# Optimization experiments

Measured on AMD Instinct MI355X. Metric: run time of the kernel, lower is better.

## Reference

```python
import jax, jax.numpy as jnp
import numpy as np

B, S, D, H, L, V = 32, 100, 1024, 16, 2, 32000
DF = 4 * D
EPS_LN = 1e-5
EPS_Q = 1e-6


def _ln(x, scale, bias):
    mu = jnp.mean(x, axis=-1, keepdims=True)
    var = jnp.mean(jnp.square(x - mu), axis=-1, keepdims=True)
    return (x - mu) * jax.lax.rsqrt(var + EPS_LN) * scale + bias


def setup_inputs() -> dict:
    key = jax.random.key(0)
    ks = jax.random.split(key, 20)
    sd = 0.02
    inp = {
        "x": jax.random.randint(ks[0], (B, S), 0, V),
        "emb": jax.random.normal(ks[1], (V, D), jnp.float32) * sd,
        "pos_emb": jax.random.normal(ks[2], (100, D), jnp.float32) * sd,
        "qkv_w": jax.random.normal(ks[3], (L, 3 * D, D), jnp.float32) * sd,
        "qkv_b": jnp.zeros((L, 3 * D), jnp.float32),
        "out_w": jax.random.normal(ks[4], (L, D, D), jnp.float32) * sd,
        "out_b": jnp.zeros((L, D), jnp.float32),
        "ln1_s": jnp.ones((L, D), jnp.float32),
        "ln1_b": jnp.zeros((L, D), jnp.float32),
        "ff1_w": jax.random.normal(ks[5], (L, DF, D), jnp.float32) * sd,
        "ff1_b": jnp.zeros((L, DF), jnp.float32),
        "ff2_w": jax.random.normal(ks[6], (L, D, DF), jnp.float32) * sd,
        "ff2_b": jnp.zeros((L, D), jnp.float32),
        "ln2_s": jnp.ones((L, D), jnp.float32),
        "ln2_b": jnp.zeros((L, D), jnp.float32),
        "dec_w": jax.random.normal(ks[7], (V, D), jnp.float32) * sd,
        "dec_b": jnp.zeros((V,), jnp.float32),
    }
    return inp


def reference(x, emb, pos_emb, qkv_w, qkv_b, out_w, out_b, ln1_s, ln1_b,
              ff1_w, ff1_b, ff2_w, ff2_b, ln2_s, ln2_b, dec_w, dec_b):
    hd = D // H
    h = emb[x] + pos_emb[:S][None, :, :]  # [B,S,D]
    for l in range(L):
        qkv = h @ qkv_w[l].T + qkv_b[l]  # [B,S,3D]
        q, k, v = jnp.split(qkv, 3, axis=-1)
        q = q.reshape(B, S, H, hd).transpose(0, 2, 1, 3)
        k = k.reshape(B, S, H, hd).transpose(0, 2, 1, 3)
        v = v.reshape(B, S, H, hd).transpose(0, 2, 1, 3)
        scores = jnp.einsum('bhqd,bhkd->bhqk', q, k) / jnp.sqrt(jnp.float32(hd))
        attn = jax.nn.softmax(scores, axis=-1)
        ctx = jnp.einsum('bhqk,bhkd->bhqd', attn, v)
        ctx = ctx.transpose(0, 2, 1, 3).reshape(B, S, D)
        attn_out = ctx @ out_w[l].T + out_b[l]
        h = _ln(h + attn_out, ln1_s[l], ln1_b[l])  # post-norm
        ff = jax.nn.gelu(h @ ff1_w[l].T + ff1_b[l], approximate=False) @ ff2_w[l].T + ff2_b[l]
        h = _ln(h + ff, ln2_s[l], ln2_b[l])
    # Ternary decoder (faithful to the original pack/unpack semantics:
    # packed code = q+1; unpack adds x when code==1 (q==0) and subtracts when
    # code==2 (q==+1), i.e. effective weight = {q==0: +1, q==+1: -1, q==-1: 0}).
    g = jnp.mean(jnp.abs(dec_w))
    wq = jnp.clip(jnp.round(dec_w / (g + EPS_Q)), -1.0, 1.0)
    w_eff = jnp.where(wq == 0.0, 1.0, jnp.where(wq == 1.0, -1.0, 0.0)).astype(jnp.float32)
    return h @ w_eff.T + dec_b  # [B,S,V]
```

## Files before the change

### kernel.cpp

```cpp
#include <hip/hip_runtime.h>
#include <hip/hip_bf16.h>
#include <math.h>

#define B_ 32
#define S_ 100
#define D_ 1024
#define H_ 16
#define L_ 2
#define V_ 32000
#define DF_ 4096
#define HD_ 64
#define MPAD 3328

typedef __bf16 bf16x8 __attribute__((ext_vector_type(8)));
typedef float f32x4 __attribute__((ext_vector_type(4)));

__device__ __forceinline__ void async_copy16(const void* g, void* l) {
  __builtin_amdgcn_global_load_lds((const __attribute__((address_space(1))) void*)g,
                                   (__attribute__((address_space(3))) void*)l, 16, 0, 0);
}

__global__ void absmean_kernel(const float* __restrict__ w, double* __restrict__ out) {
  const long long n4 = (long long)V_ * D_ / 4;
  double s = 0.0;
  long long stride = (long long)gridDim.x * blockDim.x;
  for (long long i = (long long)blockIdx.x * blockDim.x + threadIdx.x; i < n4; i += stride) {
    float4 v = ((const float4*)w)[i];
    s += (double)fabsf(v.x) + (double)fabsf(v.y) + (double)fabsf(v.z) + (double)fabsf(v.w);
  }
#pragma unroll
  for (int off = 32; off > 0; off >>= 1) s += __shfl_down(s, off);
  __shared__ double sm[4];
  int lane = threadIdx.x & 63, wv = threadIdx.x >> 6;
  if (lane == 0) sm[wv] = s;
  __syncthreads();
  if (threadIdx.x == 0) atomicAdd(out, sm[0] + sm[1] + sm[2] + sm[3]);
}

__global__ void quantize_kernel(const float* __restrict__ w, const double* __restrict__ gsum,
                                __hip_bfloat16* __restrict__ q) {
  const long long n4 = (long long)V_ * D_ / 4;
  double g = (*gsum) / ((double)V_ * D_) + 1e-6;
  long long stride = (long long)gridDim.x * blockDim.x;
  for (long long i = (long long)blockIdx.x * blockDim.x + threadIdx.x; i < n4; i += stride) {
    float4 v = ((const float4*)w)[i];
    union { __hip_bfloat16 h[4]; uint2 u; } o;
    float vv[4] = {v.x, v.y, v.z, v.w};
#pragma unroll
    for (int j = 0; j < 4; ++j) {
      double r = rint((double)vv[j] / g);
      r = fmin(1.0, fmax(-1.0, r));
      float w_eff = (r == 0.0) ? 1.0f : ((r == 1.0) ? -1.0f : 0.0f);
      o.h[j] = __float2bfloat16(w_eff);
    }
    ((uint2*)q)[i] = o.u;
  }
}

__global__ void cast_kernel(const float* __restrict__ in, __hip_bfloat16* __restrict__ out,
                            long long n4) {
  long long stride = (long long)gridDim.x * blockDim.x;
  for (long long i = (long long)blockIdx.x * blockDim.x + threadIdx.x; i < n4; i += stride) {
    float4 v = ((const float4*)in)[i];
    union { __hip_bfloat16 h[4]; uint2 u; } o;
    o.h[0] = __float2bfloat16(v.x);
    o.h[1] = __float2bfloat16(v.y);
    o.h[2] = __float2bfloat16(v.z);
    o.h[3] = __float2bfloat16(v.w);
    ((uint2*)out)[i] = o.u;
  }
}

__global__ __launch_bounds__(256) void embed_kernel(const int* __restrict__ x,
    const float* __restrict__ emb, const float* __restrict__ pos,
    float* __restrict__ h, __hip_bfloat16* __restrict__ hb) {
  int row = blockIdx.x;
  int s = row % S_;
  int tok = x[row];
  size_t eb = (size_t)tok * D_, pb = (size_t)s * D_, hb0 = (size_t)row * D_;
#pragma unroll
  for (int i = 0; i < 4; ++i) {
    int d = threadIdx.x + i * 256;
    float v = emb[eb + d] + pos[pb + d];
    h[hb0 + d] = v;
    hb[hb0 + d] = __float2bfloat16(v);
  }
}

__device__ __forceinline__ float gelu_exact(float v) {
  return 0.5f * v * (1.0f + erff(v * 0.70710678118654752f));
}

template <int ACT, int OUTBF>
__global__ __launch_bounds__(256) void gemm_bf(const __hip_bfloat16* __restrict__ A,
    const __hip_bfloat16* __restrict__ Bm, const float* __restrict__ bias,
    void* __restrict__ C, void* __restrict__ C2, int M, int N, int K, int lda, int ldb) {
  __shared__ __bf16 As[128 * 32];
  __shared__ __bf16 Bs[128 * 32];
  int tid = threadIdx.x;
  int lane = tid & 63, wid = tid >> 6;
  int wr = wid >> 1, wc = wid & 1;
  int z = blockIdx.z;

  int nwg = gridDim.x * gridDim.y;
  int orig = blockIdx.y * gridDim.x + blockIdx.x;
  int q = nwg >> 3, r = nwg & 7;
  int xcd = orig & 7, local = orig >> 3;
  int wgid = (xcd < r ? xcd * (q + 1) : r * (q + 1) + (xcd - r) * q) + local;
  int row0 = (wgid % gridDim.x) * 128;
  int col0 = (wgid / gridDim.x) * 128;

  const __hip_bfloat16* Az = A + (size_t)z * K;
  const __hip_bfloat16* Bz = Bm + (size_t)z * K;
  int j0 = wid * 2;
  const __hip_bfloat16* Ag0 = Az + (size_t)(row0 + j0 * 16 + (lane >> 2)) * lda + (lane & 3) * 8;
  const __hip_bfloat16* Ag1 = Az + (size_t)(row0 + (j0 + 1) * 16 + (lane >> 2)) * lda + (lane & 3) * 8;
  const __hip_bfloat16* Bg0 = Bz + (size_t)(col0 + j0 * 16 + (lane >> 2)) * ldb + (lane & 3) * 8;
  const __hip_bfloat16* Bg1 = Bz + (size_t)(col0 + (j0 + 1) * 16 + (lane >> 2)) * ldb + (lane & 3) * 8;
  __bf16* Al0 = As + j0 * 512;
  __bf16* Al1 = As + (j0 + 1) * 512;
  __bf16* Bl0 = Bs + j0 * 512;
  __bf16* Bl1 = Bs + (j0 + 1) * 512;

  float bias_v[4];
#pragma unroll
  for (int ni = 0; ni < 4; ++ni)
    bias_v[ni] = (z == 0) ? bias[col0 + wc * 64 + ni * 16 + (lane & 15)] : 0.f;

  f32x4 acc[4][4];
#pragma unroll
  for (int mi = 0; mi < 4; ++mi)
#pragma unroll
    for (int ni = 0; ni < 4; ++ni) acc[mi][ni] = (f32x4){0.f, 0.f, 0.f, 0.f};

  const bf16x8* Asv = reinterpret_cast<const bf16x8*>(As);
  const bf16x8* Bsv = reinterpret_cast<const bf16x8*>(Bs);
  int afr = (wr * 64 + (lane & 15)) * 4 + (lane >> 4);
  int bfr = (wc * 64 + (lane & 15)) * 4 + (lane >> 4);

  for (int k0 = 0; k0 < K; k0 += 32) {
    async_copy16(Ag0, Al0);
    async_copy16(Ag1, Al1);
    async_copy16(Bg0, Bl0);
    async_copy16(Bg1, Bl1);
    Ag0 += 32; Ag1 += 32; Bg0 += 32; Bg1 += 32;
    __syncthreads();
    bf16x8 af[4], bf[4];
#pragma unroll
    for (int mi = 0; mi < 4; ++mi) af[mi] = Asv[afr + mi * 64];
#pragma unroll
    for (int ni = 0; ni < 4; ++ni) bf[ni] = Bsv[bfr + ni * 64];
#pragma unroll
    for (int mi = 0; mi < 4; ++mi)
#pragma unroll
      for (int ni = 0; ni < 4; ++ni)
        acc[mi][ni] = __builtin_amdgcn_mfma_f32_16x16x32_bf16(af[mi], bf[ni], acc[mi][ni], 0, 0, 0);
    __syncthreads();
  }

  float* Cf = (float*)((z == 0) ? C : C2);
  __hip_bfloat16* Cb = (__hip_bfloat16*)C;
#pragma unroll
  for (int mi = 0; mi < 4; ++mi) {
#pragma unroll
    for (int r2 = 0; r2 < 4; ++r2) {
      size_t m = row0 + wr * 64 + mi * 16 + (lane >> 4) * 4 + r2;
#pragma unroll
      for (int ni = 0; ni < 4; ++ni) {
        size_t n = col0 + wc * 64 + ni * 16 + (lane & 15);
        float v = acc[mi][ni][r2] + bias_v[ni];
        if (ACT == 1) v = gelu_exact(v);
        if (OUTBF) Cb[m * N + n] = __float2bfloat16(v);
        else       Cf[m * N + n] = v;
      }
    }
  }
}

__global__ __launch_bounds__(512, 1) void gemm256_dec(
    const __hip_bfloat16* __restrict__ A, const __hip_bfloat16* __restrict__ Bm,
    const float* __restrict__ bias, float* __restrict__ C,
    int Mreal, int N, int K) {
  extern __shared__ char lds[];
  char* ldsA = lds;
  char* ldsB = lds + 65536;
  const int t = threadIdx.x;
  const int lane = t & 63, wid = t >> 6;
  const int wm = wid >> 2, wn = wid & 3;
  const int NT = K >> 6;

  int nwg = gridDim.x * gridDim.y;
  int orig = blockIdx.y * gridDim.x + blockIdx.x;
  int q = nwg >> 3, r = nwg & 7;
  int xcd = orig & 7, local = orig >> 3;
  int wgid = (xcd < r ? xcd * (q + 1) : r * (q + 1) + (xcd - r) * q) + local;
  int row0 = (wgid % gridDim.x) * 256;
  int col0 = (wgid / gridDim.x) * 256;

  const int rs = t >> 2;
  const int kc = ((((t & 3) << 4) ^ (((t >> 5) & 1) << 5)) >> 1);
  const __hip_bfloat16* Asrc = A + (size_t)(row0 + rs) * K + kc;
  const __hip_bfloat16* Bsrc = Bm + (size_t)(col0 + rs) * K + kc;

#define STAGE_A(b, h, tgt) do { \
    const __hip_bfloat16* _s = Asrc + (size_t)(h) * 128 * K + (tgt) * 64; \
    char* _d = ldsA + (b) * 32768 + (h) * 16384 + t * 16; \
    async_copy16(_s, _d); async_copy16(_s + 32, _d + 8192); } while (0)
#define STAGE_B(b, h, tgt) do { \
    const __hip_bfloat16* _s = Bsrc + (size_t)(h) * 128 * K + (tgt) * 64; \
    char* _d = ldsB + (b) * 32768 + (h) * 16384 + t * 16; \
    async_copy16(_s, _d); async_copy16(_s + 32, _d + 8192); } while (0)
#define SB() __builtin_amdgcn_sched_barrier(0)
#define BAR() __builtin_amdgcn_s_barrier()

  const int sb5 = ((lane >> 3) & 1) << 5;
  const int laneoff = ((lane & 15) << 6) + (((lane >> 4) << 4) ^ sb5);

  f32x4 acc[8][4];
#pragma unroll
  for (int i = 0; i < 8; ++i)
#pragma unroll
    for (int j = 0; j < 4; ++j) acc[i][j] = (f32x4){0.f, 0.f, 0.f, 0.f};

  STAGE_A(0, 0, 0); STAGE_B(0, 0, 0); STAGE_A(0, 1, 0); STAGE_B(0, 1, 0);
  STAGE_B(1, 0, 1); STAGE_A(1, 0, 1);
  asm volatile("s_waitcnt vmcnt(4)" ::: "memory");
  SB(); BAR(); SB();

  bf16x8 a[4][2], b[4][2];
  for (int T = 0; T < NT; ++T) {
    const int bs = T & 1;
    const char* Aw = ldsA + bs * 32768 + wm * 16384 + laneoff;
    const char* Bw = ldsB + bs * 32768 + (wn >> 1) * 16384 + (wn & 1) * 4096 + laneoff;
#pragma unroll
    for (int mi = 0; mi < 4; ++mi)
#pragma unroll
      for (int kk = 0; kk < 2; ++kk)
        a[mi][kk] = *(const bf16x8*)(Aw + mi * 1024 + kk * 8192);
#pragma unroll
    for (int ni = 0; ni < 2; ++ni)
#pragma unroll
      for (int kk = 0; kk < 2; ++kk)
        b[ni][kk] = *(const bf16x8*)(Bw + ni * 1024 + kk * 8192);
    if (T + 1 < NT) STAGE_A(bs ^ 1, 1, T + 1);
    SB(); BAR(); SB();
    __builtin_amdgcn_s_setprio(1);
#pragma unroll
    for (int mi = 0; mi < 4; ++mi)
#pragma unroll
      for (int ni = 0; ni < 2; ++ni)
#pragma unroll
        for (int kk = 0; kk < 2; ++kk)
          acc[mi][ni] = __builtin_amdgcn_mfma_f32_16x16x32_bf16(a[mi][kk], b[ni][kk], acc[mi][ni], 0, 0, 0);
    __builtin_amdgcn_s_setprio(0);
    SB(); BAR(); SB();
#pragma unroll
    for (int ni = 2; ni < 4; ++ni)
#pragma unroll
      for (int kk = 0; kk < 2; ++kk)
        b[ni][kk] = *(const bf16x8*)(Bw + ni * 1024 + kk * 8192);
    if (T + 1 < NT) STAGE_B(bs ^ 1, 1, T + 1);
    SB(); BAR(); SB();
    __builtin_amdgcn_s_setprio(1);
#pragma unroll
    for (int mi = 0; mi < 4; ++mi)
#pragma unroll
      for (int ni = 2; ni < 4; ++ni)
#pragma unroll
        for (int kk = 0; kk < 2; ++kk)
          acc[mi][ni] = __builtin_amdgcn_mfma_f32_16x16x32_bf16(a[mi][kk], b[ni][kk], acc[mi][ni], 0, 0, 0);
    __builtin_amdgcn_s_setprio(0);
    SB(); BAR(); SB();
#pragma unroll
    for (int mi = 0; mi < 4; ++mi)
#pragma unroll
      for (int kk = 0; kk < 2; ++kk)
        a[mi][kk] = *(const bf16x8*)(Aw + (mi + 4) * 1024 + kk * 8192);
    if (T + 2 < NT) STAGE_B(bs, 0, T + 2);
    SB(); BAR(); SB();
    __builtin_amdgcn_s_setprio(1);
#pragma unroll
    for (int mi = 0; mi < 4; ++mi)
#pragma unroll
      for (int ni = 0; ni < 2; ++ni)
#pragma unroll
        for (int kk = 0; kk < 2; ++kk)
          acc[mi + 4][ni] = __builtin_amdgcn_mfma_f32_16x16x32_bf16(a[mi][kk], b[ni][kk], acc[mi + 4][ni], 0, 0, 0);
    __builtin_amdgcn_s_setprio(0);
    SB(); BAR(); SB();
    if (T + 2 < NT) STAGE_A(bs, 0, T + 2);
    if (T < NT - 2) { asm volatile("s_waitcnt vmcnt(4)" ::: "memory"); }
    else            { asm volatile("s_waitcnt vmcnt(0)" ::: "memory"); }
    SB(); BAR(); SB();
    __builtin_amdgcn_s_setprio(1);
#pragma unroll
    for (int mi = 0; mi < 4; ++mi)
#pragma unroll
      for (int ni = 2; ni < 4; ++ni)
#pragma unroll
        for (int kk = 0; kk < 2; ++kk)
          acc[mi + 4][ni] = __builtin_amdgcn_mfma_f32_16x16x32_bf16(a[mi][kk], b[ni][kk], acc[mi + 4][ni], 0, 0, 0);
    __builtin_amdgcn_s_setprio(0);
    SB(); BAR(); SB();
  }
#undef STAGE_A
#undef STAGE_B
#undef SB
#undef BAR

  float bias_v[4];
#pragma unroll
  for (int ni = 0; ni < 4; ++ni)
    bias_v[ni] = bias[col0 + wn * 64 + ni * 16 + (lane & 15)];
#pragma unroll
  for (int mi = 0; mi < 8; ++mi) {
#pragma unroll
    for (int r2 = 0; r2 < 4; ++r2) {
      int m = row0 + wm * 128 + mi * 16 + (lane >> 4) * 4 + r2;
      if (m < Mreal) {
#pragma unroll
        for (int ni = 0; ni < 4; ++ni) {
          int n = col0 + wn * 64 + ni * 16 + (lane & 15);
          C[(size_t)m * N + n] = acc[mi][ni][r2] + bias_v[ni];
        }
      }
    }
  }
}

__global__ __launch_bounds__(128) void attn_kernel(const __hip_bfloat16* __restrict__ qkv,
                                                   __hip_bfloat16* __restrict__ ctx) {
  __shared__ float KV[50][64];
  __shared__ float Sc[100][100];
  int bh = blockIdx.x;
  int b = bh >> 4, hh = bh & 15;
  int tid = threadIdx.x;
  size_t base = (size_t)b * S_ * (3 * D_);
  int hcol = hh * HD_;
  int r = tid;

  float qa[64];
  if (r < 100) {
    const __hip_bfloat16* qp = qkv + base + (size_t)r * (3 * D_) + hcol;
#pragma unroll
    for (int d0 = 0; d0 < 8; ++d0) {
      union { uint4 u; __hip_bfloat16 h[8]; } uu;
      uu.u = *(const uint4*)(qp + d0 * 8);
#pragma unroll
      for (int j = 0; j < 8; ++j) qa[d0 * 8 + j] = __bfloat162float(uu.h[j]);
    }
  }
  for (int tt = 0; tt < 2; ++tt) {
    __syncthreads();
    for (int idx = tid; idx < 400; idx += 128) {
      int j = idx >> 3, d8 = idx & 7;
      union { uint4 u; __hip_bfloat16 h[8]; } uu;
      uu.u = *(const uint4*)(qkv + base + (size_t)(tt * 50 + j) * (3 * D_) + D_ + hcol + d8 * 8);
#pragma unroll
      for (int e = 0; e < 8; ++e) KV[j][d8 * 8 + e] = __bfloat162float(uu.h[e]);
    }
    __syncthreads();
    if (r < 100) {
      for (int j = 0; j < 50; ++j) {
        float s = 0.f;
#pragma unroll
        for (int d0 = 0; d0 < 16; ++d0) {
          float4 kv = *(const float4*)&KV[j][d0 * 4];
          s += qa[d0 * 4 + 0] * kv.x + qa[d0 * 4 + 1] * kv.y +
               qa[d0 * 4 + 2] * kv.z + qa[d0 * 4 + 3] * kv.w;
        }
        Sc[r][tt * 50 + j] = s * 0.125f;
      }
    }
  }
  float inv_sum = 0.f;
  if (r < 100) {
    float mx = -1e30f;
    for (int j = 0; j < 100; ++j) mx = fmaxf(mx, Sc[r][j]);
    float sum = 0.f;
    for (int j = 0; j < 100; ++j) {
      float e = expf(Sc[r][j] - mx);
      Sc[r][j] = e;
      sum += e;
    }
    inv_sum = 1.0f / sum;
  }
  float ca[64];
#pragma unroll
  for (int d = 0; d < 64; ++d) ca[d] = 0.f;
  for (int tt = 0; tt < 2; ++tt) {
    __syncthreads();
    for (int idx = tid; idx < 400; idx += 128) {
      int j = idx >> 3, d8 = idx & 7;
      union { uint4 u; __hip_bfloat16 h[8]; } uu;
      uu.u = *(const uint4*)(qkv + base + (size_t)(tt * 50 + j) * (3 * D_) + 2 * D_ + hcol + d8 * 8);
#pragma unroll
      for (int e = 0; e < 8; ++e) KV[j][d8 * 8 + e] = __bfloat162float(uu.h[e]);
    }
    __syncthreads();
    if (r < 100) {
      for (int j = 0; j < 50; ++j) {
        float p = Sc[r][tt * 50 + j];
#pragma unroll
        for (int d0 = 0; d0 < 16; ++d0) {
          float4 kv = *(const float4*)&KV[j][d0 * 4];
          ca[d0 * 4 + 0] += p * kv.x;
          ca[d0 * 4 + 1] += p * kv.y;
          ca[d0 * 4 + 2] += p * kv.z;
          ca[d0 * 4 + 3] += p * kv.w;
        }
      }
    }
  }
  if (r < 100) {
    __hip_bfloat16* cp = ctx + ((size_t)b * S_ + r) * D_ + hcol;
#pragma unroll
    for (int d = 0; d < 64; ++d) cp[d] = __float2bfloat16(ca[d] * inv_sum);
  }
}

__device__ float block_sum_1024(float v) {
#pragma unroll
  for (int off = 32; off > 0; off >>= 1) v += __shfl_down(v, off);
  __shared__ float sm[4];
  __syncthreads();
  int lane = threadIdx.x & 63, wv = threadIdx.x >> 6;
  if (lane == 0) sm[wv] = v;
  __syncthreads();
  return sm[0] + sm[1] + sm[2] + sm[3];
}

__global__ __launch_bounds__(256) void add_ln_kernel(float* __restrict__ h,
    const float* __restrict__ res, const float* __restrict__ res2,
    const float* __restrict__ scale, const float* __restrict__ bias,
    __hip_bfloat16* __restrict__ hb) {
  size_t base = (size_t)blockIdx.x * D_;
  int tid = threadIdx.x;
  float x[4];
  float s = 0.f;
#pragma unroll
  for (int i = 0; i < 4; ++i) {
    size_t ix = base + tid + i * 256;
    float v = h[ix] + res[ix];
    if (res2) v += res2[ix];
    x[i] = v;
    s += v;
  }
  float mu = block_sum_1024(s) * (1.0f / 1024.0f);
  float v = 0.f;
#pragma unroll
  for (int i = 0; i < 4; ++i) {
    float d = x[i] - mu;
    v += d * d;
  }
  float var = block_sum_1024(v) * (1.0f / 1024.0f);
  float rs = rsqrtf(var + 1e-5f);
#pragma unroll
  for (int i = 0; i < 4; ++i) {
    int d = tid + i * 256;
    float o = (x[i] - mu) * rs * scale[d] + bias[d];
    h[base + d] = o;
    hb[base + d] = __float2bfloat16(o);
  }
}

extern "C" void kernel_launch(void* const* d_in, const int* in_sizes, int n_in,
                              void* d_out, int out_size, void* d_ws, size_t ws_size,
                              hipStream_t stream) {
  const int* x       = (const int*)d_in[0];
  const float* emb   = (const float*)d_in[1];
  const float* pos   = (const float*)d_in[2];
  const float* qkv_w = (const float*)d_in[3];
  const float* qkv_b = (const float*)d_in[4];
  const float* out_w = (const float*)d_in[5];
  const float* out_b = (const float*)d_in[6];
  const float* ln1_s = (const float*)d_in[7];
  const float* ln1_b = (const float*)d_in[8];
  const float* ff1_w = (const float*)d_in[9];
  const float* ff1_b = (const float*)d_in[10];
  const float* ff2_w = (const float*)d_in[11];
  const float* ff2_b = (const float*)d_in[12];
  const float* ln2_s = (const float*)d_in[13];
  const float* ln2_b = (const float*)d_in[14];
  const float* dec_w = (const float*)d_in[15];
  const float* dec_b = (const float*)d_in[16];
  float* out = (float*)d_out;

  char* ws = (char*)d_ws;
  size_t off = 0;
  auto alloc = [&](size_t bytes) { void* p = ws + off; off += (bytes + 255) & ~(size_t)255; return p; };
  double* gsum            = (double*)alloc(256);
  float* h                = (float*)alloc((size_t)3200 * 1024 * 4);
  __hip_bfloat16* h_bf    = (__hip_bfloat16*)alloc((size_t)MPAD * 1024 * 2);
  float* tmp              = (float*)alloc((size_t)3200 * 1024 * 4);
  float* tmp2             = (float*)alloc((size_t)3200 * 1024 * 4);
  __hip_bfloat16* ctx_bf  = (__hip_bfloat16*)alloc((size_t)3200 * 1024 * 2);
  __hip_bfloat16* big_bf  = (__hip_bfloat16*)alloc((size_t)3200 * 4096 * 2);
  __hip_bfloat16* weff    = (__hip_bfloat16*)alloc((size_t)32000 * 1024 * 2);
  __hip_bfloat16* qkvw_bf = (__hip_bfloat16*)alloc((size_t)2 * 3072 * 1024 * 2);
  __hip_bfloat16* outw_bf = (__hip_bfloat16*)alloc((size_t)2 * 1024 * 1024 * 2);
  __hip_bfloat16* ff1w_bf = (__hip_bfloat16*)alloc((size_t)2 * 4096 * 1024 * 2);
  __hip_bfloat16* ff2w_bf = (__hip_bfloat16*)alloc((size_t)2 * 1024 * 4096 * 2);

  hipMemsetAsync(gsum, 0, 256, stream);
  absmean_kernel<<<2048, 256, 0, stream>>>(dec_w, gsum);
  quantize_kernel<<<4096, 256, 0, stream>>>(dec_w, gsum, weff);
  cast_kernel<<<2048, 256, 0, stream>>>(qkv_w, qkvw_bf, (long long)2 * 3072 * 1024 / 4);
  cast_kernel<<<2048, 256, 0, stream>>>(out_w, outw_bf, (long long)2 * 1024 * 1024 / 4);
  cast_kernel<<<2048, 256, 0, stream>>>(ff1_w, ff1w_bf, (long long)2 * 4096 * 1024 / 4);
  cast_kernel<<<2048, 256, 0, stream>>>(ff2_w, ff2w_bf, (long long)2 * 1024 * 4096 / 4);
  embed_kernel<<<3200, 256, 0, stream>>>(x, emb, pos, h, h_bf);

  const int M = 3200;
  for (int l = 0; l < 2; ++l) {
    gemm_bf<0, 1><<<dim3(M / 128, 3072 / 128, 1), 256, 0, stream>>>(
        h_bf, qkvw_bf + (size_t)l * 3072 * 1024, qkv_b + l * 3072, big_bf, nullptr,
        M, 3072, 1024, 1024, 1024);
    attn_kernel<<<512, 128, 0, stream>>>(big_bf, ctx_bf);
    gemm_bf<0, 0><<<dim3(M / 128, 1024 / 128, 2), 256, 0, stream>>>(
        ctx_bf, outw_bf + (size_t)l * 1024 * 1024, out_b + l * 1024, tmp, tmp2,
        M, 1024, 512, 1024, 1024);
    add_ln_kernel<<<M, 256, 0, stream>>>(h, tmp, tmp2, ln1_s + l * 1024, ln1_b + l * 1024, h_bf);
    gemm_bf<1, 1><<<dim3(M / 128, 4096 / 128, 1), 256, 0, stream>>>(
        h_bf, ff1w_bf + (size_t)l * 4096 * 1024, ff1_b + l * 4096, big_bf, nullptr,
        M, 4096, 1024, 1024, 1024);
    gemm_bf<0, 0><<<dim3(M / 128, 1024 / 128, 2), 256, 0, stream>>>(
        big_bf, ff2w_bf + (size_t)l * 1024 * 4096, ff2_b + l * 1024, tmp, tmp2,
        M, 1024, 2048, 4096, 4096);
    add_ln_kernel<<<M, 256, 0, stream>>>(h, tmp, tmp2, ln2_s + l * 1024, ln2_b + l * 1024, h_bf);
  }
  gemm256_dec<<<dim3(MPAD / 256, 32000 / 256), 512, 131072, stream>>>(
      h_bf, weff, dec_b, out, M, 32000, 1024);
}
```

Measured before the change: 981.1 us.

## Double GEMM K-tile, fuse weight casts, vectorize add-LN, pad attention scores

The bf16 GEMM now stages a 64-wide K slice per iteration instead of 32, which halves the number of barrier pairs and runs twice as many MFMAs between them. The four weight-cast launches are merged into one kernel that indexes across all four tensors. add_ln loads and stores with float4 (the element-to-thread mapping changes, which is safe because the reduction is over the whole row). The attention score buffer is padded to 101 columns to avoid LDS bank conflicts. The larger LDS footprint and extra registers in the GEMM may lower occupancy.

```diff
diff --git a/kernel.cpp b/kernel.cpp
--- a/kernel.cpp
+++ b/kernel.cpp
@@ -57,17 +57,28 @@
   }
 }
 
-__global__ void cast_kernel(const float* __restrict__ in, __hip_bfloat16* __restrict__ out,
-                            long long n4) {
+__global__ void cast_all_kernel(const float* __restrict__ qkv_w, const float* __restrict__ out_w,
+                                const float* __restrict__ ff1_w, const float* __restrict__ ff2_w,
+                                __hip_bfloat16* __restrict__ qd, __hip_bfloat16* __restrict__ od,
+                                __hip_bfloat16* __restrict__ f1d, __hip_bfloat16* __restrict__ f2d) {
+  const long long n1 = (long long)2 * 3072 * 1024 / 4;
+  const long long n2 = n1 + (long long)2 * 1024 * 1024 / 4;
+  const long long n3 = n2 + (long long)2 * 4096 * 1024 / 4;
+  const long long n4 = n3 + (long long)2 * 1024 * 4096 / 4;
   long long stride = (long long)gridDim.x * blockDim.x;
   for (long long i = (long long)blockIdx.x * blockDim.x + threadIdx.x; i < n4; i += stride) {
-    float4 v = ((const float4*)in)[i];
+    const float* src; __hip_bfloat16* dst; long long j;
+    if (i < n1)      { src = qkv_w; dst = qd;  j = i; }
+    else if (i < n2) { src = out_w; dst = od;  j = i - n1; }
+    else if (i < n3) { src = ff1_w; dst = f1d; j = i - n2; }
+    else             { src = ff2_w; dst = f2d; j = i - n3; }
+    float4 v = ((const float4*)src)[j];
     union { __hip_bfloat16 h[4]; uint2 u; } o;
     o.h[0] = __float2bfloat16(v.x);
     o.h[1] = __float2bfloat16(v.y);
     o.h[2] = __float2bfloat16(v.z);
     o.h[3] = __float2bfloat16(v.w);
-    ((uint2*)out)[i] = o.u;
+    ((uint2*)dst)[j] = o.u;
   }
 }
 
@@ -95,8 +106,8 @@
 __global__ __launch_bounds__(256) void gemm_bf(const __hip_bfloat16* __restrict__ A,
     const __hip_bfloat16* __restrict__ Bm, const float* __restrict__ bias,
     void* __restrict__ C, void* __restrict__ C2, int M, int N, int K, int lda, int ldb) {
-  __shared__ __bf16 As[128 * 32];
-  __shared__ __bf16 Bs[128 * 32];
+  __shared__ __bf16 As[128 * 64];
+  __shared__ __bf16 Bs[128 * 64];
   int tid = threadIdx.x;
   int lane = tid & 63, wid = tid >> 6;
   int wr = wid >> 1, wc = wid & 1;
@@ -138,23 +149,29 @@
   int afr = (wr * 64 + (lane & 15)) * 4 + (lane >> 4);
   int bfr = (wc * 64 + (lane & 15)) * 4 + (lane >> 4);
 
-  for (int k0 = 0; k0 < K; k0 += 32) {
-    async_copy16(Ag0, Al0);
-    async_copy16(Ag1, Al1);
-    async_copy16(Bg0, Bl0);
-    async_copy16(Bg1, Bl1);
-    Ag0 += 32; Ag1 += 32; Bg0 += 32; Bg1 += 32;
+  for (int k0 = 0; k0 < K; k0 += 64) {
+    async_copy16(Ag0, Al0);  async_copy16(Ag0 + 32, (char*)Al0 + 8192);
+    async_copy16(Ag1, Al1);  async_copy16(Ag1 + 32, (char*)Al1 + 8192);
+    async_copy16(Bg0, Bl0);  async_copy16(Bg0 + 32, (char*)Bl0 + 8192);
+    async_copy16(Bg1, Bl1);  async_copy16(Bg1 + 32, (char*)Bl1 + 8192);
+    Ag0 += 64; Ag1 += 64; Bg0 += 64; Bg1 += 64;
     __syncthreads();
-    bf16x8 af[4], bf[4];
-#pragma unroll
-    for (int mi = 0; mi < 4; ++mi) af[mi] = Asv[afr + mi * 64];
-#pragma unroll
-    for (int ni = 0; ni < 4; ++ni) bf[ni] = Bsv[bfr + ni * 64];
+    bf16x8 af[4][2], bq[4][2];
+#pragma unroll
+    for (int mi = 0; mi < 4; ++mi)
+#pragma unroll
+      for (int kk = 0; kk < 2; ++kk) af[mi][kk] = Asv[afr + mi * 64 + kk * 512];
+#pragma unroll
+    for (int ni = 0; ni < 4; ++ni)
+#pragma unroll
+      for (int kk = 0; kk < 2; ++kk) bq[ni][kk] = Bsv[bfr + ni * 64 + kk * 512];
 #pragma unroll
     for (int mi = 0; mi < 4; ++mi)
 #pragma unroll
       for (int ni = 0; ni < 4; ++ni)
-        acc[mi][ni] = __builtin_amdgcn_mfma_f32_16x16x32_bf16(af[mi], bf[ni], acc[mi][ni], 0, 0, 0);
+#pragma unroll
+        for (int kk = 0; kk < 2; ++kk)
+          acc[mi][ni] = __builtin_amdgcn_mfma_f32_16x16x32_bf16(af[mi][kk], bq[ni][kk], acc[mi][ni], 0, 0, 0);
     __syncthreads();
   }
 
@@ -331,7 +348,7 @@
 __global__ __launch_bounds__(128) void attn_kernel(const __hip_bfloat16* __restrict__ qkv,
                                                    __hip_bfloat16* __restrict__ ctx) {
   __shared__ float KV[50][64];
-  __shared__ float Sc[100][100];
+  __shared__ float Sc[100][101];
   int bh = blockIdx.x;
   int b = bh >> 4, hh = bh & 15;
   int tid = threadIdx.x;
@@ -434,18 +451,15 @@
     const float* __restrict__ res, const float* __restrict__ res2,
     const float* __restrict__ scale, const float* __restrict__ bias,
     __hip_bfloat16* __restrict__ hb) {
-  size_t base = (size_t)blockIdx.x * D_;
-  int tid = threadIdx.x;
-  float x[4];
-  float s = 0.f;
-#pragma unroll
-  for (int i = 0; i < 4; ++i) {
-    size_t ix = base + tid + i * 256;
-    float v = h[ix] + res[ix];
-    if (res2) v += res2[ix];
-    x[i] = v;
-    s += v;
-  }
+  size_t b4 = (size_t)blockIdx.x * 256 + threadIdx.x;
+  float4 xa = ((const float4*)h)[b4];
+  float4 xb = ((const float4*)res)[b4];
+  float x[4] = {xa.x + xb.x, xa.y + xb.y, xa.z + xb.z, xa.w + xb.w};
+  if (res2) {
+    float4 xc = ((const float4*)res2)[b4];
+    x[0] += xc.x; x[1] += xc.y; x[2] += xc.z; x[3] += xc.w;
+  }
+  float s = x[0] + x[1] + x[2] + x[3];
   float mu = block_sum_1024(s) * (1.0f / 1024.0f);
   float v = 0.f;
 #pragma unroll
@@ -455,13 +469,19 @@
   }
   float var = block_sum_1024(v) * (1.0f / 1024.0f);
   float rs = rsqrtf(var + 1e-5f);
-#pragma unroll
-  for (int i = 0; i < 4; ++i) {
-    int d = tid + i * 256;
-    float o = (x[i] - mu) * rs * scale[d] + bias[d];
-    h[base + d] = o;
-    hb[base + d] = __float2bfloat16(o);
-  }
+  int d0 = threadIdx.x * 4;
+  float4 sc = *(const float4*)&scale[d0];
+  float4 bi = *(const float4*)&bias[d0];
+  float o[4];
+  o[0] = (x[0] - mu) * rs * sc.x + bi.x;
+  o[1] = (x[1] - mu) * rs * sc.y + bi.y;
+  o[2] = (x[2] - mu) * rs * sc.z + bi.z;
+  o[3] = (x[3] - mu) * rs * sc.w + bi.w;
+  ((float4*)h)[b4] = (float4){o[0], o[1], o[2], o[3]};
+  union { __hip_bfloat16 hh[4]; uint2 u; } ob;
+#pragma unroll
+  for (int i = 0; i < 4; ++i) ob.hh[i] = __float2bfloat16(o[i]);
+  ((uint2*)hb)[b4] = ob.u;
 }
 
 extern "C" void kernel_launch(void* const* d_in, const int* in_sizes, int n_in,
@@ -505,10 +525,8 @@
   hipMemsetAsync(gsum, 0, 256, stream);
   absmean_kernel<<<2048, 256, 0, stream>>>(dec_w, gsum);
   quantize_kernel<<<4096, 256, 0, stream>>>(dec_w, gsum, weff);
-  cast_kernel<<<2048, 256, 0, stream>>>(qkv_w, qkvw_bf, (long long)2 * 3072 * 1024 / 4);
-  cast_kernel<<<2048, 256, 0, stream>>>(out_w, outw_bf, (long long)2 * 1024 * 1024 / 4);
-  cast_kernel<<<2048, 256, 0, stream>>>(ff1_w, ff1w_bf, (long long)2 * 4096 * 1024 / 4);
-  cast_kernel<<<2048, 256, 0, stream>>>(ff2_w, ff2w_bf, (long long)2 * 1024 * 4096 / 4);
+  cast_all_kernel<<<4096, 256, 0, stream>>>(qkv_w, out_w, ff1_w, ff2_w,
+                                            qkvw_bf, outw_bf, ff1w_bf, ff2w_bf);
   embed_kernel<<<3200, 256, 0, stream>>>(x, emb, pos, h, h_bf);
 
   const int M = 3200;
```

New measurement: 924.9 us. -5.7%, faster.
